# Kernel optimization log

Hardware: AMD Instinct MI355X
Metric: run time of the kernel (lower is better)

The kernel has to match this reference:

```python
import jax, jax.numpy as jnp
import numpy as np

B, N, C, H = 8, 2048, 1024, 16
D = C // H
FOCUSING_FACTOR = 3
KERNEL = 5
EPS_BN = 1e-5


def setup_inputs() -> dict:
    key = jax.random.key(0)
    ks = jax.random.split(key, 6)
    s = lambda k, shape: jax.random.normal(k, shape, dtype=jnp.float32) * 0.02
    return {
        "hidden_states": jax.random.normal(ks[0], (B, N, C), dtype=jnp.float32),
        "bn_gamma": jnp.ones((C,), jnp.float32),
        "bn_beta": jnp.zeros((C,), jnp.float32),
        "W_qkv": s(ks[1], (C, 3 * C)),
        "b_qkv": jnp.zeros((3 * C,), jnp.float32),
        "scale_p": jnp.zeros((1, 1, C), jnp.float32),
        "dwc_w": s(ks[2], (C, 1, KERNEL)),
        "dwc_b": jnp.zeros((C,), jnp.float32),
        "W_proj": s(ks[3], (C, C)),
        "b_proj": jnp.zeros((C,), jnp.float32),
    }


def _focus(t, scale):
    # Focused feature map: relu kernel, scale, then power-3 sharpening with norm restoration
    t = jax.nn.relu(t) + 1e-6
    t = t / scale
    nrm = jnp.linalg.norm(t, axis=-1, keepdims=True)
    t = t ** FOCUSING_FACTOR
    return t / jnp.linalg.norm(t, axis=-1, keepdims=True) * nrm


def reference(hidden_states, bn_gamma, bn_beta, W_qkv, b_qkv, scale_p, dwc_w, dwc_b, W_proj, b_proj):
    x = hidden_states  # (B, N, C)
    # BatchNorm1d in training mode: per-channel stats over batch and sequence
    mean = jnp.mean(x, axis=(0, 1))
    var = jnp.mean((x - mean) ** 2, axis=(0, 1))  # biased, as torch BN uses
    xn = (x - mean) * jax.lax.rsqrt(var + EPS_BN) * bn_gamma + bn_beta

    qkv = xn @ W_qkv + b_qkv
    q, k, v = jnp.split(qkv, 3, axis=-1)
    scale = jax.nn.softplus(scale_p)
    q = _focus(q, scale)
    k = _focus(k, scale)

    heads = lambda t: t.reshape(B, N, H, D).transpose(0, 2, 1, 3)  # (B,H,N,D)
    qh, kh, vh = heads(q), heads(k), heads(v)

    # Linear attention: O(N*D^2) instead of O(N^2*D)
    z = 1.0 / (jnp.einsum('bhnd,bhd->bhn', qh, kh.sum(axis=2)) + 1e-6)
    kv = jnp.einsum('bhnd,bhne->bhde', kh, vh)  # (B,H,D,D)
    o = jnp.einsum('bhnd,bhde->bhne', qh, kv) * z[..., None]
    o = o.transpose(0, 2, 1, 3).reshape(B, N, C)

    # Depthwise conv residual on v over the sequence dim
    vc = v.transpose(0, 2, 1)  # (B,C,N)
    dwc = jax.lax.conv_general_dilated(
        vc, dwc_w, window_strides=(1,), padding=[(KERNEL // 2, KERNEL // 2)],
        dimension_numbers=('NCH', 'OIH', 'NCH'), feature_group_count=C)
    dwc = (dwc + dwc_b[None, :, None]).transpose(0, 2, 1)

    return (o + dwc) @ W_proj + b_proj
```

## Files before the change

### kernel.cpp

```cpp
#include <hip/hip_runtime.h>


#define DEV __device__ __forceinline__

typedef __attribute__((ext_vector_type(8))) short bf16x8;
typedef __attribute__((ext_vector_type(4))) float f32x4;
typedef unsigned short us;

DEV float bf2f(us u) {
  union { unsigned int i; float f; } v; v.i = ((unsigned int)u) << 16; return v.f;
}
DEV us f2bf(float f) {
  union { float f; unsigned int i; } v; v.f = f;
  unsigned int r = v.i + 0x7FFFu + ((v.i >> 16) & 1u);
  return (us)(r >> 16);
}
DEV void glds16(const us* g, us* l) {
  __builtin_amdgcn_global_load_lds((const __attribute__((address_space(1))) unsigned int*)g,
                                   (__attribute__((address_space(3))) unsigned int*)l, 16, 0, 0);
}

#define MEMFENCE asm volatile("" ::: "memory")

__global__ void zero_f32(float* p, int n) {
  int i = blockIdx.x * 256 + threadIdx.x;
  if (i < n) p[i] = 0.f;
}

__global__ __launch_bounds__(256) void bn_stats(const float* __restrict__ x,
                                                float* __restrict__ s_sum, float* __restrict__ s_sq) {
  int t = threadIdx.x;
  int c0 = t * 4;
  size_t row0 = (size_t)blockIdx.x * 64;
  float s[4] = {0.f,0.f,0.f,0.f}, q[4] = {0.f,0.f,0.f,0.f};
  for (int r = 0; r < 64; ++r) {
    f32x4 v = *(const f32x4*)&x[(row0 + r) * 1024 + c0];
    #pragma unroll
    for (int i = 0; i < 4; ++i) { float f = v[i]; s[i] += f; q[i] += f * f; }
  }
  #pragma unroll
  for (int i = 0; i < 4; ++i) { atomicAdd(&s_sum[c0 + i], s[i]); atomicAdd(&s_sq[c0 + i], q[i]); }
}

__global__ void bn_finalize(const float* __restrict__ s_sum, const float* __restrict__ s_sq,
                            const float* __restrict__ gamma, const float* __restrict__ beta,
                            const float* __restrict__ scalep,
                            float* __restrict__ bn_a, float* __restrict__ bn_b, float* __restrict__ invs) {
  int c = threadIdx.x;
  float mean = s_sum[c] * (1.0f / 16384.0f);
  float var  = s_sq[c] * (1.0f / 16384.0f) - mean * mean;
  float a = gamma[c] * rsqrtf(var + 1e-5f);
  bn_a[c] = a;
  bn_b[c] = beta[c] - mean * a;
  float sv = scalep[c];
  float sp = (sv > 20.f) ? sv : log1pf(expf(sv));
  invs[c] = 1.0f / sp;
}

__global__ __launch_bounds__(256) void xn_to_bf16(const float* __restrict__ x,
                                                  const float* __restrict__ bn_a, const float* __restrict__ bn_b,
                                                  us* __restrict__ xn) {
  size_t base = ((size_t)blockIdx.x * 256 + threadIdx.x) * 8;
  int c = (int)(base & 1023);
  f32x4 a0 = *(const f32x4*)&x[base];
  f32x4 a1 = *(const f32x4*)&x[base + 4];
  uint4 o; us* uo = (us*)&o;
  #pragma unroll
  for (int i = 0; i < 4; ++i) uo[i] = f2bf(bn_a[c + i] * a0[i] + bn_b[c + i]);
  #pragma unroll
  for (int i = 0; i < 4; ++i) uo[4 + i] = f2bf(bn_a[c + 4 + i] * a1[i] + bn_b[c + 4 + i]);
  *(uint4*)&xn[base] = o;
}

__global__ __launch_bounds__(256) void transpose_f32_bf16(const float* __restrict__ in,
                                                          us* __restrict__ out, int R, int Cc) {
  __shared__ float tile[64 * 65];
  int tx = blockIdx.x * 64, ty = blockIdx.y * 64;
  int t = threadIdx.x;
  {
    int rr = t >> 4, g = t & 15;
    #pragma unroll
    for (int p = 0; p < 4; ++p) {
      int r = p * 16 + rr;
      f32x4 v = *(const f32x4*)&in[(size_t)(ty + r) * Cc + tx + g * 4];
      #pragma unroll
      for (int i = 0; i < 4; ++i) tile[r * 65 + g * 4 + i] = v[i];
    }
  }
  __syncthreads();
  {
    int rr = t >> 3, g = t & 7;
    #pragma unroll
    for (int p = 0; p < 2; ++p) {
      int nl = p * 32 + rr;
      uint4 v; us* u = (us*)&v;
      #pragma unroll
      for (int j = 0; j < 8; ++j) u[j] = f2bf(tile[(g * 8 + j) * 65 + nl]);
      *(uint4*)&out[(size_t)(tx + nl) * R + ty + g * 8] = v;
    }
  }
}

template <typename OutT>
__global__ __launch_bounds__(512, 2) void gemm256(const us* __restrict__ A,
                                                  const us* __restrict__ Bt,
                                                  const float* __restrict__ bias,
                                                  OutT* __restrict__ Ca,
                                                  OutT* __restrict__ Cb) {
  constexpr int GK = 1024;
  __shared__ __align__(16) us As[4][128 * 64];
  __shared__ __align__(16) us Bs[4][128 * 64];
  int t = threadIdx.x;
  int wid = t >> 6, lane = t & 63;
  int l16 = lane & 15, qd = lane >> 4;
  int nwx = gridDim.x;
  int id = blockIdx.y * nwx + blockIdx.x;
  int nwg = nwx * (int)gridDim.y;
  int sw = (id & 7) * (nwg >> 3) + (id >> 3);
  int n0 = (sw % nwx) * 256, m0 = (sw / nwx) * 256;

  int rr = lane >> 3, sl = lane & 7;
  int lg = sl ^ rr;
  int grp = lg >> 2, ch = lg & 3;
  const us* Abase = A + (size_t)(m0 + wid * 8 + rr + 128 * grp) * GK + ch * 8;
  const us* Bbase = Bt + (size_t)(n0 + wid * 8 + rr + 128 * grp) * GK + ch * 8;
  us* lA = (us*)&As[0][0] + (wid * 8) * 64;
  us* lB = (us*)&Bs[0][0] + (wid * 8) * 64;

  int amG = wid & 1;
  int wn = (wid >> 1) * 64;

  f32x4 acc[8][4];
  const f32x4 zero4 = {0.f, 0.f, 0.f, 0.f};
  #pragma unroll
  for (int i = 0; i < 8; ++i)
    #pragma unroll
    for (int j = 0; j < 4; ++j) acc[i][j] = zero4;

  auto STAGE = [&](int kt) {
    int b = kt & 3;
    const us* sa = Abase + kt * 32;
    const us* sb = Bbase + kt * 32;
    #pragma unroll
    for (int p = 0; p < 2; ++p) {
      glds16(sa + (size_t)p * 64 * GK, lA + b * 8192 + p * 64 * 64);
      glds16(sb + (size_t)p * 64 * GK, lB + b * 8192 + p * 64 * 64);
    }
  };

  auto BODY = [&](int kt) {
    int b = kt & 3;
    bf16x8 af[8], bfr[4];
    #pragma unroll
    for (int i = 0; i < 8; ++i) {
      int ra = i * 16 + l16;
      int ph = (amG * 4 + qd) ^ (l16 & 7);
      af[i] = *(const bf16x8*)&As[b][ra * 64 + ph * 8];
    }
    #pragma unroll
    for (int j = 0; j < 4; ++j) {
      int nr = wn + j * 16;
      int rb = (nr & 127) + l16;
      int ph = ((nr >> 7) * 4 + qd) ^ (l16 & 7);
      bfr[j] = *(const bf16x8*)&Bs[b][rb * 64 + ph * 8];
    }
    __builtin_amdgcn_s_setprio(1);
    #pragma unroll
    for (int i = 0; i < 8; ++i)
      #pragma unroll
      for (int j = 0; j < 4; ++j)
        acc[i][j] = __builtin_amdgcn_mfma_f32_16x16x32_bf16(af[i], bfr[j], acc[i][j], 0, 0, 0);
    __builtin_amdgcn_s_setprio(0);
  };

  STAGE(0); STAGE(1); STAGE(2);

  for (int kt = 0; kt < 29; ++kt) {
    asm volatile("s_waitcnt vmcnt(8)" ::: "memory");
    MEMFENCE; __builtin_amdgcn_s_barrier(); MEMFENCE;
    STAGE(kt + 3);
    BODY(kt);
  }
  asm volatile("s_waitcnt vmcnt(8)" ::: "memory");
  MEMFENCE; __builtin_amdgcn_s_barrier(); MEMFENCE;
  BODY(29);
  asm volatile("s_waitcnt vmcnt(4)" ::: "memory");
  MEMFENCE; __builtin_amdgcn_s_barrier(); MEMFENCE;
  BODY(30);
  asm volatile("s_waitcnt vmcnt(0)" ::: "memory");
  MEMFENCE; __builtin_amdgcn_s_barrier(); MEMFENCE;
  BODY(31);

  OutT* Cp; int col0;
  if (n0 < 1024) { Cp = Ca; col0 = n0; } else { Cp = Cb; col0 = n0 - 1024; }
  #pragma unroll
  for (int i = 0; i < 8; ++i) {
    int row = m0 + amG * 128 + i * 16 + qd * 4;
    #pragma unroll
    for (int j = 0; j < 4; ++j) {
      int fc = n0 + wn + j * 16 + l16;
      float bv = bias[fc];
      int col = col0 + wn + j * 16 + l16;
      #pragma unroll
      for (int r = 0; r < 4; ++r) {
        float val = acc[i][j][r] + bv;
        if constexpr (sizeof(OutT) == 2)
          ((us*)Cp)[(size_t)(row + r) * 1024 + col] = f2bf(val);
        else
          ((float*)Cp)[(size_t)(row + r) * 1024 + col] = val;
      }
    }
  }
}

__global__ __launch_bounds__(256) void focus_kernel(us* __restrict__ buf,
                                                    const float* __restrict__ invs) {
  int row = blockIdx.x;
  us* p = buf + (size_t)row * 1024;
  int t = threadIdx.x;
  int c0 = t * 4;
  uint2 v = *(uint2*)&p[c0];
  us* u = (us*)&v;
  float ti[4]; float s2 = 0.f, s6 = 0.f;
  #pragma unroll
  for (int i = 0; i < 4; ++i) {
    float f = bf2f(u[i]);
    f = fmaxf(f, 0.f) + 1e-6f;
    f *= invs[c0 + i];
    ti[i] = f;
    float f2 = f * f;
    s2 += f2; s6 += f2 * f2 * f2;
  }
  #pragma unroll
  for (int off = 32; off > 0; off >>= 1) { s2 += __shfl_down(s2, off); s6 += __shfl_down(s6, off); }
  __shared__ float red[8]; __shared__ float bc;
  int wid = t >> 6, lane = t & 63;
  if (lane == 0) { red[wid] = s2; red[4 + wid] = s6; }
  __syncthreads();
  if (t == 0) {
    float a = red[0] + red[1] + red[2] + red[3];
    float b2 = red[4] + red[5] + red[6] + red[7];
    bc = sqrtf(a / b2);
  }
  __syncthreads();
  float factor = bc;
  #pragma unroll
  for (int i = 0; i < 4; ++i) u[i] = f2bf(ti[i] * ti[i] * ti[i] * factor);
  *(uint2*)&p[c0] = v;
}

__global__ __launch_bounds__(256) void attn_stats3(const us* __restrict__ kbuf,
                                                   const us* __restrict__ vbuf,
                                                   float* __restrict__ ksum,
                                                   float* __restrict__ kvpart) {
  int cx = blockIdx.x, h = blockIdx.y, b = blockIdx.z, bh = b * 16 + h;
  int t = threadIdx.x, wid = t >> 6, lane = t & 63;
  int l16 = lane & 15, qd = lane >> 4;
  int wm = (wid & 1) * 32, wn = (wid >> 1) * 32;
  __shared__ __align__(16) us kT[64 * 80];
  __shared__ __align__(16) us vT[64 * 80];
  const f32x4 zero4 = {0.f, 0.f, 0.f, 0.f};
  f32x4 acc[2][2];
  #pragma unroll
  for (int i = 0; i < 2; ++i)
    #pragma unroll
    for (int j = 0; j < 2; ++j) acc[i][j] = zero4;
  float ksacc = 0.f;
  int np = (t & 31) * 2, ch0 = (t >> 5) * 8;

  for (int ck = 0; ck < 4; ++ck) {
    __syncthreads();
    size_t base = ((size_t)b * 2048 + cx * 256 + ck * 64 + np) * 1024 + h * 64 + ch0;
    uint4 k0 = *(const uint4*)&kbuf[base];
    uint4 k1 = *(const uint4*)&kbuf[base + 1024];
    uint4 v0 = *(const uint4*)&vbuf[base];
    uint4 v1 = *(const uint4*)&vbuf[base + 1024];
    us* pk0 = (us*)&k0; us* pk1 = (us*)&k1; us* pv0 = (us*)&v0; us* pv1 = (us*)&v1;
    #pragma unroll
    for (int i = 0; i < 8; ++i) {
      unsigned int pk = (unsigned int)pk0[i] | ((unsigned int)pk1[i] << 16);
      unsigned int pv = (unsigned int)pv0[i] | ((unsigned int)pv1[i] << 16);
      *(unsigned int*)&kT[(ch0 + i) * 80 + np] = pk;
      *(unsigned int*)&vT[(ch0 + i) * 80 + np] = pv;
    }
    __syncthreads();
    if (t < 64) {
      #pragma unroll
      for (int g = 0; g < 8; ++g) {
        bf16x8 kk = *(const bf16x8*)&kT[t * 80 + g * 8];
        #pragma unroll
        for (int j = 0; j < 8; ++j) ksacc += bf2f(((us*)&kk)[j]);
      }
    }
    #pragma unroll
    for (int ks = 0; ks < 2; ++ks) {
      bf16x8 af[2], bfr[2];
      #pragma unroll
      for (int i = 0; i < 2; ++i) {
        af[i]  = *(const bf16x8*)&kT[(wm + i * 16 + l16) * 80 + ks * 32 + qd * 8];
        bfr[i] = *(const bf16x8*)&vT[(wn + i * 16 + l16) * 80 + ks * 32 + qd * 8];
      }
      #pragma unroll
      for (int i = 0; i < 2; ++i)
        #pragma unroll
        for (int j = 0; j < 2; ++j)
          acc[i][j] = __builtin_amdgcn_mfma_f32_16x16x32_bf16(af[i], bfr[j], acc[i][j], 0, 0, 0);
    }
  }
  float* pp = kvpart + ((size_t)cx * 128 + bh) * 4096;
  #pragma unroll
  for (int i = 0; i < 2; ++i) {
    int d = wm + i * 16 + qd * 4;
    #pragma unroll
    for (int j = 0; j < 2; ++j) {
      int e = wn + j * 16 + l16;
      #pragma unroll
      for (int r = 0; r < 4; ++r) pp[(d + r) * 64 + e] = acc[i][j][r];
    }
  }
  if (t < 64) atomicAdd(&ksum[bh * 64 + t], ksacc);
}

__global__ __launch_bounds__(256) void kv_reduce(const float* __restrict__ part, us* __restrict__ kvT) {
  int bh = blockIdx.x;
  int t = threadIdx.x;
  __shared__ float kvl[4096];
  #pragma unroll
  for (int p = 0; p < 16; ++p) {
    int i = p * 256 + t;
    float s = 0.f;
    #pragma unroll
    for (int c = 0; c < 8; ++c) s += part[((size_t)c * 128 + bh) * 4096 + i];
    kvl[i] = s;
  }
  __syncthreads();
  #pragma unroll
  for (int p = 0; p < 2; ++p) {
    int idx = p * 256 + t;
    int e = idx >> 3, d0 = (idx & 7) * 8;
    uint4 o; us* uo = (us*)&o;
    #pragma unroll
    for (int i = 0; i < 8; ++i) uo[i] = f2bf(kvl[(d0 + i) * 64 + e]);
    *(uint4*)&kvT[(size_t)bh * 4096 + e * 64 + d0] = o;
  }
}

__global__ __launch_bounds__(256) void attn_o2(us* __restrict__ qod,
                                               const us* __restrict__ vbuf,
                                               const float* __restrict__ ksum,
                                               const us* __restrict__ kvT,
                                               const float* __restrict__ dwcw,
                                               const float* __restrict__ dwcb) {
  int nt = blockIdx.x, h = blockIdx.y, b = blockIdx.z, bh = b * 16 + h;
  int t = threadIdx.x, wid = t >> 6, lane = t & 63;
  int l16 = lane & 15, qd = lane >> 4;
  __shared__ __align__(16) us qs[128 * 64];
  __shared__ __align__(16) us bs[64 * 64];
  __shared__ __align__(16) us vs[132 * 64];
  __shared__ float zl[128];
  __shared__ float ksl[64];
  __shared__ float wl[64 * 5];
  __shared__ float bl[64];
  int rS = t >> 3, gS = t & 7;
  size_t qbase = ((size_t)b * 2048 + nt * 128) * 1024 + h * 64;
  #pragma unroll
  for (int p = 0; p < 4; ++p) {
    int r = p * 32 + rS;
    uint4 v = *(const uint4*)&qod[qbase + (size_t)r * 1024 + gS * 8];
    *(uint4*)&qs[r * 64 + ((gS ^ (r & 7)) * 8)] = v;
  }
  #pragma unroll
  for (int p = 0; p < 2; ++p) {
    int r = p * 32 + rS;
    uint4 v = *(const uint4*)&kvT[(size_t)bh * 4096 + r * 64 + gS * 8];
    *(uint4*)&bs[r * 64 + ((gS ^ (r & 7)) * 8)] = v;
  }
  int n0 = nt * 128;
  #pragma unroll
  for (int p = 0; p < 5; ++p) {
    int idx = p * 256 + t;
    if (idx < 1056) {
      int r = idx >> 3, g = idx & 7;
      int n = n0 - 2 + r;
      uint4 v = make_uint4(0, 0, 0, 0);
      if (n >= 0 && n < 2048)
        v = *(const uint4*)&vbuf[((size_t)b * 2048 + n) * 1024 + h * 64 + g * 8];
      *(uint4*)&vs[r * 64 + g * 8] = v;
    }
  }
  if (t < 64) {
    ksl[t] = ksum[bh * 64 + t];
    bl[t] = dwcb[h * 64 + t];
    #pragma unroll
    for (int j = 0; j < 5; ++j) wl[t * 5 + j] = dwcw[(h * 64 + t) * 5 + j];
  }
  __syncthreads();
  if (t < 128) {
    float zs = 0.f;
    #pragma unroll
    for (int g = 0; g < 8; ++g) {
      bf16x8 qv = *(const bf16x8*)&qs[t * 64 + ((g ^ (t & 7)) * 8)];
      #pragma unroll
      for (int j = 0; j < 8; ++j) zs += bf2f(((us*)&qv)[j]) * ksl[g * 8 + j];
    }
    zl[t] = 1.f / (zs + 1e-6f);
  }
  __syncthreads();
  const f32x4 zero4 = {0.f, 0.f, 0.f, 0.f};
  f32x4 acc[2][4];
  #pragma unroll
  for (int i = 0; i < 2; ++i)
    #pragma unroll
    for (int j = 0; j < 4; ++j) acc[i][j] = zero4;
  #pragma unroll
  for (int ks = 0; ks < 2; ++ks) {
    bf16x8 af[2], bfr[4];
    #pragma unroll
    for (int i = 0; i < 2; ++i) {
      int ml = (wid * 2 + i) * 16 + l16;
      af[i] = *(const bf16x8*)&qs[ml * 64 + (((ks * 4 + qd) ^ (ml & 7)) * 8)];
    }
    #pragma unroll
    for (int j = 0; j < 4; ++j) {
      int nl = j * 16 + l16;
      bfr[j] = *(const bf16x8*)&bs[nl * 64 + (((ks * 4 + qd) ^ (nl & 7)) * 8)];
    }
    #pragma unroll
    for (int i = 0; i < 2; ++i)
      #pragma unroll
      for (int j = 0; j < 4; ++j)
        acc[i][j] = __builtin_amdgcn_mfma_f32_16x16x32_bf16(af[i], bfr[j], acc[i][j], 0, 0, 0);
  }
  #pragma unroll
  for (int i = 0; i < 2; ++i) {
    int rl0 = (wid * 2 + i) * 16 + qd * 4;
    #pragma unroll
    for (int j = 0; j < 4; ++j) {
      int e = j * 16 + l16;
      float w0 = wl[e * 5], w1 = wl[e * 5 + 1], w2 = wl[e * 5 + 2], w3 = wl[e * 5 + 3], w4 = wl[e * 5 + 4];
      float vv[8];
      #pragma unroll
      for (int m = 0; m < 8; ++m) vv[m] = bf2f(vs[(rl0 + m) * 64 + e]);
      float bb = bl[e];
      #pragma unroll
      for (int r = 0; r < 4; ++r) {
        float dwc = vv[r] * w0 + vv[r + 1] * w1 + vv[r + 2] * w2 + vv[r + 3] * w3 + vv[r + 4] * w4;
        float o = acc[i][j][r] * zl[rl0 + r] + dwc + bb;
        qod[qbase + (size_t)(rl0 + r) * 1024 + e] = f2bf(o);
      }
    }
  }
}

extern "C" void kernel_launch(void* const* d_in, const int* in_sizes, int n_in,
                              void* d_out, int out_size, void* d_ws, size_t ws_size,
                              hipStream_t stream) {
  const float* x      = (const float*)d_in[0];
  const float* gamma  = (const float*)d_in[1];
  const float* beta   = (const float*)d_in[2];
  const float* Wqkv   = (const float*)d_in[3];
  const float* bqkv   = (const float*)d_in[4];
  const float* scalep = (const float*)d_in[5];
  const float* dwcw   = (const float*)d_in[6];
  const float* dwcb   = (const float*)d_in[7];
  const float* Wproj  = (const float*)d_in[8];
  const float* bproj  = (const float*)d_in[9];
  float* out = (float*)d_out;

  float* wsf = (float*)d_ws;
  float* s_sum  = wsf;
  float* s_sq   = wsf + 1024;
  float* ksum   = wsf + 2048;
  float* bn_a   = wsf + 10240;
  float* bn_b   = wsf + 11264;
  float* invs   = wsf + 12288;
  float* kvpart = wsf + 13312;
  us* kvT = (us*)(wsf + 4207616);
  us* wtq = (us*)(wsf + 4469760);
  us* wtp = (us*)(wsf + 6042624);
  us* kq  = (us*)(wsf + 6566912);
  us* vbf = (us*)d_out;
  us* xnb = (us*)d_out + 16777216;

  zero_f32<<<40, 256, 0, stream>>>(wsf, 10240);
  bn_stats<<<256, 256, 0, stream>>>(x, s_sum, s_sq);
  bn_finalize<<<1, 1024, 0, stream>>>(s_sum, s_sq, gamma, beta, scalep, bn_a, bn_b, invs);
  xn_to_bf16<<<8192, 256, 0, stream>>>(x, bn_a, bn_b, xnb);
  transpose_f32_bf16<<<dim3(48, 16), 256, 0, stream>>>(Wqkv, wtq, 1024, 3072);
  transpose_f32_bf16<<<dim3(16, 16), 256, 0, stream>>>(Wproj, wtp, 1024, 1024);

  gemm256<us><<<dim3(8, 64), 512, 0, stream>>>(xnb, wtq + 1024 * 1024, bqkv + 1024, kq, vbf);
  focus_kernel<<<16384, 256, 0, stream>>>(kq, invs);
  attn_stats3<<<dim3(8, 16, 8), 256, 0, stream>>>(kq, vbf, ksum, kvpart);
  kv_reduce<<<128, 256, 0, stream>>>(kvpart, kvT);
  gemm256<us><<<dim3(4, 64), 512, 0, stream>>>(xnb, wtq, bqkv, kq, kq);
  focus_kernel<<<16384, 256, 0, stream>>>(kq, invs);
  attn_o2<<<dim3(16, 16, 8), 256, 0, stream>>>(kq, vbf, ksum, kvT, dwcw, dwcb);
  gemm256<float><<<dim3(4, 64), 512, 0, stream>>>(kq, wtp, bproj, out, out);
}
```

Before: 424.9 us.

## Switch GEMM to two-stage double buffer with 64-wide K tiles

Replaces the GEMM's four-deep, 32-wide K pipeline with a two-buffer scheme that loads 64-wide K tiles, one tile ahead. This halves the number of barrier and wait points per tile. The shared-memory loads become contiguous per-wave row blocks with an XOR swizzle. The warp layout is remapped to 2x4 (row/col) tiles. The trade-off is less prefetch depth: each iteration waits for all outstanding loads (vmcnt(0)) before the next barrier, which may expose more memory latency.

```diff
diff --git a/kernel.cpp b/kernel.cpp
--- a/kernel.cpp
+++ b/kernel.cpp
@@ -108,8 +108,8 @@
                                                   OutT* __restrict__ Ca,
                                                   OutT* __restrict__ Cb) {
   constexpr int GK = 1024;
-  __shared__ __align__(16) us As[4][128 * 64];
-  __shared__ __align__(16) us Bs[4][128 * 64];
+  __shared__ __align__(16) us As[2][256 * 64];
+  __shared__ __align__(16) us Bs[2][256 * 64];
   int t = threadIdx.x;
   int wid = t >> 6, lane = t & 63;
   int l16 = lane & 15, qd = lane >> 4;
@@ -119,16 +119,13 @@
   int sw = (id & 7) * (nwg >> 3) + (id >> 3);
   int n0 = (sw % nwx) * 256, m0 = (sw / nwx) * 256;
 
-  int rr = lane >> 3, sl = lane & 7;
-  int lg = sl ^ rr;
-  int grp = lg >> 2, ch = lg & 3;
-  const us* Abase = A + (size_t)(m0 + wid * 8 + rr + 128 * grp) * GK + ch * 8;
-  const us* Bbase = Bt + (size_t)(n0 + wid * 8 + rr + 128 * grp) * GK + ch * 8;
-  us* lA = (us*)&As[0][0] + (wid * 8) * 64;
-  us* lB = (us*)&Bs[0][0] + (wid * 8) * 64;
-
-  int amG = wid & 1;
-  int wn = (wid >> 1) * 64;
+  int rr = lane >> 3, lg = (lane & 7) ^ rr;
+  const us* Abase = A + (size_t)(m0 + wid * 32 + rr) * GK + lg * 8;
+  const us* Bbase = Bt + (size_t)(n0 + wid * 32 + rr) * GK + lg * 8;
+  us* lA = (us*)&As[0][0] + (wid * 32) * 64;
+  us* lB = (us*)&Bs[0][0] + (wid * 32) * 64;
+
+  int wr = wid >> 2, wc = wid & 3;
 
   f32x4 acc[8][4];
   const f32x4 zero4 = {0.f, 0.f, 0.f, 0.f};
@@ -138,69 +135,66 @@
     for (int j = 0; j < 4; ++j) acc[i][j] = zero4;
 
   auto STAGE = [&](int kt) {
-    int b = kt & 3;
-    const us* sa = Abase + kt * 32;
-    const us* sb = Bbase + kt * 32;
-    #pragma unroll
-    for (int p = 0; p < 2; ++p) {
-      glds16(sa + (size_t)p * 64 * GK, lA + b * 8192 + p * 64 * 64);
-      glds16(sb + (size_t)p * 64 * GK, lB + b * 8192 + p * 64 * 64);
+    int b = kt & 1;
+    const us* sa = Abase + kt * 64;
+    const us* sb = Bbase + kt * 64;
+    #pragma unroll
+    for (int g = 0; g < 4; ++g) {
+      glds16(sa + (size_t)g * 8 * GK, lA + b * 16384 + g * 8 * 64);
+      glds16(sb + (size_t)g * 8 * GK, lB + b * 16384 + g * 8 * 64);
     }
   };
 
   auto BODY = [&](int kt) {
-    int b = kt & 3;
-    bf16x8 af[8], bfr[4];
-    #pragma unroll
-    for (int i = 0; i < 8; ++i) {
-      int ra = i * 16 + l16;
-      int ph = (amG * 4 + qd) ^ (l16 & 7);
-      af[i] = *(const bf16x8*)&As[b][ra * 64 + ph * 8];
-    }
-    #pragma unroll
-    for (int j = 0; j < 4; ++j) {
-      int nr = wn + j * 16;
-      int rb = (nr & 127) + l16;
-      int ph = ((nr >> 7) * 4 + qd) ^ (l16 & 7);
-      bfr[j] = *(const bf16x8*)&Bs[b][rb * 64 + ph * 8];
-    }
-    __builtin_amdgcn_s_setprio(1);
-    #pragma unroll
-    for (int i = 0; i < 8; ++i)
-      #pragma unroll
-      for (int j = 0; j < 4; ++j)
-        acc[i][j] = __builtin_amdgcn_mfma_f32_16x16x32_bf16(af[i], bfr[j], acc[i][j], 0, 0, 0);
-    __builtin_amdgcn_s_setprio(0);
+    int b = kt & 1;
+    #pragma unroll
+    for (int ks = 0; ks < 2; ++ks) {
+      bf16x8 af[8], bfr[4];
+      #pragma unroll
+      for (int i = 0; i < 8; ++i) {
+        int r = wr * 128 + i * 16 + l16;
+        int sl = (ks * 4 + qd) ^ (r & 7);
+        af[i] = *(const bf16x8*)&As[b][r * 64 + sl * 8];
+      }
+      #pragma unroll
+      for (int j = 0; j < 4; ++j) {
+        int r = wc * 64 + j * 16 + l16;
+        int sl = (ks * 4 + qd) ^ (r & 7);
+        bfr[j] = *(const bf16x8*)&Bs[b][r * 64 + sl * 8];
+      }
+      __builtin_amdgcn_s_setprio(1);
+      #pragma unroll
+      for (int i = 0; i < 8; ++i)
+        #pragma unroll
+        for (int j = 0; j < 4; ++j)
+          acc[i][j] = __builtin_amdgcn_mfma_f32_16x16x32_bf16(af[i], bfr[j], acc[i][j], 0, 0, 0);
+      __builtin_amdgcn_s_setprio(0);
+    }
   };
 
-  STAGE(0); STAGE(1); STAGE(2);
-
-  for (int kt = 0; kt < 29; ++kt) {
-    asm volatile("s_waitcnt vmcnt(8)" ::: "memory");
-    MEMFENCE; __builtin_amdgcn_s_barrier(); MEMFENCE;
-    STAGE(kt + 3);
-    BODY(kt);
-  }
-  asm volatile("s_waitcnt vmcnt(8)" ::: "memory");
-  MEMFENCE; __builtin_amdgcn_s_barrier(); MEMFENCE;
-  BODY(29);
-  asm volatile("s_waitcnt vmcnt(4)" ::: "memory");
-  MEMFENCE; __builtin_amdgcn_s_barrier(); MEMFENCE;
-  BODY(30);
+  STAGE(0);
   asm volatile("s_waitcnt vmcnt(0)" ::: "memory");
   MEMFENCE; __builtin_amdgcn_s_barrier(); MEMFENCE;
-  BODY(31);
+
+  for (int kt = 0; kt < 16; ++kt) {
+    if (kt + 1 < 16) STAGE(kt + 1);
+    BODY(kt);
+    if (kt + 1 < 16) {
+      asm volatile("s_waitcnt vmcnt(0)" ::: "memory");
+      MEMFENCE; __builtin_amdgcn_s_barrier(); MEMFENCE;
+    }
+  }
 
   OutT* Cp; int col0;
   if (n0 < 1024) { Cp = Ca; col0 = n0; } else { Cp = Cb; col0 = n0 - 1024; }
   #pragma unroll
   for (int i = 0; i < 8; ++i) {
-    int row = m0 + amG * 128 + i * 16 + qd * 4;
+    int row = m0 + wr * 128 + i * 16 + qd * 4;
     #pragma unroll
     for (int j = 0; j < 4; ++j) {
-      int fc = n0 + wn + j * 16 + l16;
+      int fc = n0 + wc * 64 + j * 16 + l16;
       float bv = bias[fc];
-      int col = col0 + wn + j * 16 + l16;
+      int col = col0 + wc * 64 + j * 16 + l16;
       #pragma unroll
       for (int r = 0; r < 4; ++r) {
         float val = acc[i][j][r] + bv;
```

Measured after the change: 409.9 us. 3.5% less time.
